# Kernel tuning notes

Measured on AMD Instinct MI355X. Metric: run time of the kernel, lower is better.

Reference implementation:

```python
import jax, jax.numpy as jnp
import numpy as np

N = 500000
D = 128
S = 4096


def setup_inputs() -> dict:
    key = jax.random.key(0)
    ks = jax.random.split(key, 8)
    x = jax.random.normal(ks[0], (N, D), dtype=jnp.float32)
    subnet_id = jax.random.randint(ks[1], (N,), 0, S, dtype=jnp.int32)
    # MLP params (Linear(D,D) x2), LayerNorm params
    lim = 1.0 / np.sqrt(D)
    W1 = jax.random.uniform(ks[2], (D, D), minval=-lim, maxval=lim, dtype=jnp.float32)
    b1 = jax.random.uniform(ks[3], (D,), minval=-lim, maxval=lim, dtype=jnp.float32)
    W2 = jax.random.uniform(ks[4], (D, D), minval=-lim, maxval=lim, dtype=jnp.float32)
    b2 = jax.random.uniform(ks[5], (D,), minval=-lim, maxval=lim, dtype=jnp.float32)
    gamma = jnp.ones((D,), dtype=jnp.float32)
    beta = jnp.zeros((D,), dtype=jnp.float32)
    return {"x": x, "subnet_id": subnet_id, "num_subnets": S,
            "W1": W1, "b1": b1, "W2": W2, "b2": b2, "gamma": gamma, "beta": beta}


def reference(x, subnet_id, num_subnets, W1, b1, W2, b2, gamma, beta):
    # scatter-mean over subnets: [S, D]
    seg_sum = jax.ops.segment_sum(x, subnet_id, num_segments=num_subnets)
    cnt = jax.ops.segment_sum(jnp.ones((x.shape[0],), x.dtype), subnet_id,
                              num_segments=num_subnets)
    mean = seg_sum / jnp.maximum(cnt, 1.0)[:, None]
    # MLP (dropout is identity in eval)
    h = jax.nn.relu(mean @ W1 + b1) @ W2 + b2
    # gather back + residual
    out = x + h[subnet_id]
    # LayerNorm (eps=1e-5)
    mu = jnp.mean(out, axis=-1, keepdims=True)
    var = jnp.var(out, axis=-1, keepdims=True)
    return (out - mu) * jax.lax.rsqrt(var + 1e-5) * gamma + beta
```

## Files before the change

kernel.cpp:

```cpp
#include <hip/hip_runtime.h>
#include <hip/hip_bf16.h>

#define DD  128
#define SS  4096
#define CAP 256

typedef float f32x4 __attribute__((ext_vector_type(4)));

static __device__ __forceinline__ void nt_store4(float* p, const float4 v) {
    f32x4 t; t[0] = v.x; t[1] = v.y; t[2] = v.z; t[3] = v.w;
    __builtin_nontemporal_store(t, (f32x4*)p);
}

__global__ void scatter_kernel(const int* __restrict__ sid,
                               int* __restrict__ fill,
                               int* __restrict__ idx, int n) {
    const int i4 = blockIdx.x * blockDim.x + threadIdx.x;
    const int n4 = n >> 2;
    if (i4 < n4) {
        int4 v = reinterpret_cast<const int4*>(sid)[i4];
        const int base = i4 * 4;
        int p;
        p = atomicAdd(&fill[v.x], 1); if (p < CAP) idx[v.x * CAP + p] = base;
        p = atomicAdd(&fill[v.y], 1); if (p < CAP) idx[v.y * CAP + p] = base + 1;
        p = atomicAdd(&fill[v.z], 1); if (p < CAP) idx[v.z * CAP + p] = base + 2;
        p = atomicAdd(&fill[v.w], 1); if (p < CAP) idx[v.w * CAP + p] = base + 3;
    }
    const int tail0 = n4 * 4;
    const int ti = tail0 + i4;
    if (ti < n && i4 < (n - tail0)) {
        int id = sid[ti];
        int p = atomicAdd(&fill[id], 1);
        if (p < CAP) idx[id * CAP + p] = ti;
    }
}

__global__ __launch_bounds__(256) void seg_mlp_kernel(
        const float* __restrict__ x,
        const int* __restrict__ idx,
        const int* __restrict__ cnt,
        const float* __restrict__ W1,
        const float* __restrict__ b1,
        const float* __restrict__ W2,
        const float* __restrict__ b2,
        float* __restrict__ h) {
    const int s    = blockIdx.x;
    const int t    = threadIdx.x;
    const int wave = t >> 6;
    const int lane = t & 63;
    const int half = lane >> 5;
    const int sub  = lane & 31;

    __shared__ int    lidx[CAP];
    __shared__ float4 part4[8][32];
    __shared__ float  m[DD];
    __shared__ float  tmp[2][DD];

    const int c  = cnt[s];
    const int cc = (c < CAP) ? c : CAP;

    if (t < cc) lidx[t] = idx[s * CAP + t];
    __syncthreads();

    const int slot = wave * 2 + half;
    const float4* x4 = reinterpret_cast<const float4*>(x);
    float4 a0 = make_float4(0.f, 0.f, 0.f, 0.f);
    float4 a1 = make_float4(0.f, 0.f, 0.f, 0.f);
    float4 a2 = make_float4(0.f, 0.f, 0.f, 0.f);
    float4 a3 = make_float4(0.f, 0.f, 0.f, 0.f);
    int j = slot;
    for (; j + 24 < cc; j += 32) {
        const int r0 = lidx[j];
        const int r1 = lidx[j + 8];
        const int r2 = lidx[j + 16];
        const int r3 = lidx[j + 24];
        float4 v0 = x4[(size_t)r0 * 32 + sub];
        float4 v1 = x4[(size_t)r1 * 32 + sub];
        float4 v2 = x4[(size_t)r2 * 32 + sub];
        float4 v3 = x4[(size_t)r3 * 32 + sub];
        a0.x += v0.x; a0.y += v0.y; a0.z += v0.z; a0.w += v0.w;
        a1.x += v1.x; a1.y += v1.y; a1.z += v1.z; a1.w += v1.w;
        a2.x += v2.x; a2.y += v2.y; a2.z += v2.z; a2.w += v2.w;
        a3.x += v3.x; a3.y += v3.y; a3.z += v3.z; a3.w += v3.w;
    }
    for (; j < cc; j += 8) {
        float4 v0 = x4[(size_t)lidx[j] * 32 + sub];
        a0.x += v0.x; a0.y += v0.y; a0.z += v0.z; a0.w += v0.w;
    }
    a0.x += a1.x + a2.x + a3.x;
    a0.y += a1.y + a2.y + a3.y;
    a0.z += a1.z + a2.z + a3.z;
    a0.w += a1.w + a2.w + a3.w;
    part4[slot][sub] = a0;
    __syncthreads();

    if (t < DD) {
        const float* pf = (const float*)part4;
        float sum = 0.f;
#pragma unroll
        for (int p = 0; p < 8; ++p) sum += pf[p * DD + t];
        m[t] = sum / fmaxf((float)c, 1.0f);
    }
    __syncthreads();

    {
        const int col = t & 127, kh = t >> 7, k0 = kh * 64;
        float a = 0.f;
        for (int k = k0; k < k0 + 64; ++k) a = fmaf(m[k], W1[k * DD + col], a);
        tmp[kh][col] = a;
    }
    __syncthreads();
    if (t < DD) m[t] = fmaxf(tmp[0][t] + tmp[1][t] + b1[t], 0.f);
    __syncthreads();

    {
        const int col = t & 127, kh = t >> 7, k0 = kh * 64;
        float a = 0.f;
        for (int k = k0; k < k0 + 64; ++k) a = fmaf(m[k], W2[k * DD + col], a);
        tmp[kh][col] = a;
    }
    __syncthreads();
    if (t < DD) h[(size_t)s * DD + t] = tmp[0][t] + tmp[1][t] + b2[t];
}

__global__ __launch_bounds__(256) void ln_kernel(
        const float* __restrict__ x,
        const int* __restrict__ sid,
        const float* __restrict__ h,
        const float* __restrict__ gamma,
        const float* __restrict__ beta,
        float* __restrict__ out,
        int n) {
    const int wave   = (blockIdx.x * blockDim.x + threadIdx.x) >> 6;
    const int lane   = threadIdx.x & 63;
    const int rrow   = lane >> 4;
    const int rsub   = lane & 15;
    const int nwaves = (gridDim.x * blockDim.x) >> 6;

    const float4* g4 = (const float4*)gamma;
    const float4* b4 = (const float4*)beta;
    const float4 ga = g4[rsub * 2],     ba = b4[rsub * 2];
    const float4 gb = g4[rsub * 2 + 1], bb = b4[rsub * 2 + 1];

    const int ngrp = n >> 2;
    for (int grp = wave; grp < ngrp; grp += nwaves) {
        const int row = grp * 4 + rrow;
        const int id  = sid[row];
        const float4* xr = (const float4*)(x + (size_t)row * DD);
        const float4* hr = (const float4*)(h + (size_t)id * DD);
        float4 o0 = xr[rsub * 2], o1 = xr[rsub * 2 + 1];
        float4 h0 = hr[rsub * 2], h1 = hr[rsub * 2 + 1];
        o0.x += h0.x; o0.y += h0.y; o0.z += h0.z; o0.w += h0.w;
        o1.x += h1.x; o1.y += h1.y; o1.z += h1.z; o1.w += h1.w;

        float sum = ((o0.x + o0.y) + (o0.z + o0.w)) +
                    ((o1.x + o1.y) + (o1.z + o1.w));
        float sq = o0.x * o0.x;
        sq = fmaf(o0.y, o0.y, sq); sq = fmaf(o0.z, o0.z, sq);
        sq = fmaf(o0.w, o0.w, sq); sq = fmaf(o1.x, o1.x, sq);
        sq = fmaf(o1.y, o1.y, sq); sq = fmaf(o1.z, o1.z, sq);
        sq = fmaf(o1.w, o1.w, sq);
#pragma unroll
        for (int off = 8; off; off >>= 1) {
            sum += __shfl_xor(sum, off);
            sq  += __shfl_xor(sq, off);
        }
        const float mu   = sum * (1.0f / DD);
        const float var  = sq * (1.0f / DD) - mu * mu;
        const float rstd = rsqrtf(var + 1e-5f);

        float4 r0, r1;
        r0.x = (o0.x - mu) * rstd * ga.x + ba.x;
        r0.y = (o0.y - mu) * rstd * ga.y + ba.y;
        r0.z = (o0.z - mu) * rstd * ga.z + ba.z;
        r0.w = (o0.w - mu) * rstd * ga.w + ba.w;
        r1.x = (o1.x - mu) * rstd * gb.x + bb.x;
        r1.y = (o1.y - mu) * rstd * gb.y + bb.y;
        r1.z = (o1.z - mu) * rstd * gb.z + bb.z;
        r1.w = (o1.w - mu) * rstd * gb.w + bb.w;
        float* orow = out + (size_t)row * DD;
        nt_store4(orow + rsub * 8,     r0);
        nt_store4(orow + rsub * 8 + 4, r1);
    }
}

extern "C" void kernel_launch(void* const* d_in, const int* in_sizes, int n_in,
                              void* d_out, int out_size, void* d_ws, size_t ws_size,
                              hipStream_t stream) {
    const float* x     = (const float*)d_in[0];
    const int*   sid   = (const int*)d_in[1];
    const float* W1    = (const float*)d_in[3];
    const float* b1    = (const float*)d_in[4];
    const float* W2    = (const float*)d_in[5];
    const float* b2    = (const float*)d_in[6];
    const float* gamma = (const float*)d_in[7];
    const float* beta  = (const float*)d_in[8];
    float*       out   = (float*)d_out;

    const int n = in_sizes[1];

    float* h    = (float*)d_ws;
    int*   fill = (int*)(h + (size_t)SS * DD);
    int*   idx  = fill + SS;

    hipMemsetAsync(fill, 0, SS * sizeof(int), stream);

    const int n4blocks = ((n >> 2) + 255) / 256 + 1;
    scatter_kernel<<<n4blocks, 256, 0, stream>>>(sid, fill, idx, n);
    seg_mlp_kernel<<<SS, 256, 0, stream>>>(x, idx, fill, W1, b1, W2, b2, h);
    ln_kernel<<<2048, 256, 0, stream>>>(x, sid, h, gamma, beta, out, n);
}
```

Before: 207.0 us.

## Split segment mean from MLP and batch eight subnets per MLP block

The fused per-subnet kernel, which read all of W1 and W2 for every one of the 4096 subnets, becomes two kernels. One computes segment means into workspace. A separate MLP kernel handles 8 subnets per block, so each weight load is reused across 8 rows held in registers. This cuts weight traffic and lets the mean kernel finish without MLP work. The cost is an extra launch and a mean round-trip through global memory, and the MLP grid has only 512 blocks of 128 threads.

```diff
diff --git a/kernel.cpp b/kernel.cpp
--- a/kernel.cpp
+++ b/kernel.cpp
@@ -35,15 +35,11 @@
     }
 }
 
-__global__ __launch_bounds__(256) void seg_mlp_kernel(
+__global__ __launch_bounds__(256) void seg_mean_kernel(
         const float* __restrict__ x,
         const int* __restrict__ idx,
         const int* __restrict__ cnt,
-        const float* __restrict__ W1,
-        const float* __restrict__ b1,
-        const float* __restrict__ W2,
-        const float* __restrict__ b2,
-        float* __restrict__ h) {
+        float* __restrict__ mean) {
     const int s    = blockIdx.x;
     const int t    = threadIdx.x;
     const int wave = t >> 6;
@@ -53,8 +49,6 @@
 
     __shared__ int    lidx[CAP];
     __shared__ float4 part4[8][32];
-    __shared__ float  m[DD];
-    __shared__ float  tmp[2][DD];
 
     const int c  = cnt[s];
     const int cc = (c < CAP) ? c : CAP;
@@ -99,28 +93,50 @@
         float sum = 0.f;
 #pragma unroll
         for (int p = 0; p < 8; ++p) sum += pf[p * DD + t];
-        m[t] = sum / fmaxf((float)c, 1.0f);
-    }
-    __syncthreads();
-
-    {
-        const int col = t & 127, kh = t >> 7, k0 = kh * 64;
-        float a = 0.f;
-        for (int k = k0; k < k0 + 64; ++k) a = fmaf(m[k], W1[k * DD + col], a);
-        tmp[kh][col] = a;
-    }
-    __syncthreads();
-    if (t < DD) m[t] = fmaxf(tmp[0][t] + tmp[1][t] + b1[t], 0.f);
-    __syncthreads();
-
-    {
-        const int col = t & 127, kh = t >> 7, k0 = kh * 64;
-        float a = 0.f;
-        for (int k = k0; k < k0 + 64; ++k) a = fmaf(m[k], W2[k * DD + col], a);
-        tmp[kh][col] = a;
-    }
-    __syncthreads();
-    if (t < DD) h[(size_t)s * DD + t] = tmp[0][t] + tmp[1][t] + b2[t];
+        mean[(size_t)s * DD + t] = sum / fmaxf((float)c, 1.0f);
+    }
+}
+
+__global__ __launch_bounds__(128) void mlp_kernel(
+        const float* __restrict__ mean,
+        const float* __restrict__ W1,
+        const float* __restrict__ b1,
+        const float* __restrict__ W2,
+        const float* __restrict__ b2,
+        float* __restrict__ h) {
+    __shared__ float m[8][DD];
+    const int t  = threadIdx.x;
+    const int s0 = blockIdx.x * 8;
+
+#pragma unroll
+    for (int r = 0; r < 8; ++r)
+        m[r][t] = mean[(size_t)(s0 + r) * DD + t];
+    __syncthreads();
+
+    float acc[8];
+    const float bv = b1[t];
+#pragma unroll
+    for (int r = 0; r < 8; ++r) acc[r] = bv;
+    for (int k = 0; k < DD; ++k) {
+        const float w = W1[k * DD + t];
+#pragma unroll
+        for (int r = 0; r < 8; ++r) acc[r] = fmaf(m[r][k], w, acc[r]);
+    }
+    __syncthreads();
+#pragma unroll
+    for (int r = 0; r < 8; ++r) m[r][t] = fmaxf(acc[r], 0.0f);
+    __syncthreads();
+
+    const float b2v = b2[t];
+#pragma unroll
+    for (int r = 0; r < 8; ++r) acc[r] = b2v;
+    for (int k = 0; k < DD; ++k) {
+        const float w = W2[k * DD + t];
+#pragma unroll
+        for (int r = 0; r < 8; ++r) acc[r] = fmaf(m[r][k], w, acc[r]);
+    }
+#pragma unroll
+    for (int r = 0; r < 8; ++r) h[(size_t)(s0 + r) * DD + t] = acc[r];
 }
 
 __global__ __launch_bounds__(256) void ln_kernel(
@@ -200,13 +216,15 @@
     const int n = in_sizes[1];
 
     float* h    = (float*)d_ws;
-    int*   fill = (int*)(h + (size_t)SS * DD);
+    float* mean = h + (size_t)SS * DD;
+    int*   fill = (int*)(mean + (size_t)SS * DD);
     int*   idx  = fill + SS;
 
     hipMemsetAsync(fill, 0, SS * sizeof(int), stream);
 
     const int n4blocks = ((n >> 2) + 255) / 256 + 1;
     scatter_kernel<<<n4blocks, 256, 0, stream>>>(sid, fill, idx, n);
-    seg_mlp_kernel<<<SS, 256, 0, stream>>>(x, idx, fill, W1, b1, W2, b2, h);
+    seg_mean_kernel<<<SS, 256, 0, stream>>>(x, idx, fill, mean);
+    mlp_kernel<<<SS / 8, DD, 0, stream>>>(mean, W1, b1, W2, b2, h);
     ln_kernel<<<2048, 256, 0, stream>>>(x, sid, h, gamma, beta, out, n);
 }
```

Result: slower. 214.6 us (+3.7%).

## Fuse scatter, segment-mean, MLP and LayerNorm into one cooperative kernel

Applied to the files above, without the earlier changes.

Replaces the memset plus three kernel launches with a single cooperative kernel of 512 blocks that uses grid-wide syncs between the phases: zeroing counts, scattering indices, segment sums, the MLP and the LayerNorm. The MLP phase now processes 4 segment rows per thread, so each W1/W2 element loaded is reused across rows. This removes launch gaps and per-kernel tail effects. In exchange it adds four grid barriers, cuts parallelism in the segment-sum phase (8 segments per block, run in sequence), adds a workspace round trip for the means, and keeps a fallback path if the cooperative launch fails.

```diff
diff --git a/kernel.cpp b/kernel.cpp
--- a/kernel.cpp
+++ b/kernel.cpp
@@ -1,15 +1,221 @@
 #include <hip/hip_runtime.h>
 #include <hip/hip_bf16.h>
-
-#define DD  128
-#define SS  4096
-#define CAP 256
+#include <hip/hip_cooperative_groups.h>
+
+namespace cg = cooperative_groups;
+
+#define DD   128
+#define SS   4096
+#define CAP  256
+#define NBLK 512
+#define NTHR 256
 
 typedef float f32x4 __attribute__((ext_vector_type(4)));
 
 static __device__ __forceinline__ void nt_store4(float* p, const float4 v) {
     f32x4 t; t[0] = v.x; t[1] = v.y; t[2] = v.z; t[3] = v.w;
     __builtin_nontemporal_store(t, (f32x4*)p);
+}
+
+__global__ __launch_bounds__(NTHR, 4) void fused_kernel(
+        const float* __restrict__ x,
+        const int*   __restrict__ sid,
+        const float* __restrict__ W1,
+        const float* __restrict__ b1,
+        const float* __restrict__ W2,
+        const float* __restrict__ b2,
+        const float* __restrict__ gamma,
+        const float* __restrict__ beta,
+        float*       __restrict__ out,
+        float*       __restrict__ h,
+        float*       __restrict__ mean,
+        int*         __restrict__ fill,
+        int*         __restrict__ idx,
+        int n) {
+    cg::grid_group grid = cg::this_grid();
+    const int t        = threadIdx.x;
+    const int gtid     = blockIdx.x * NTHR + t;
+    const int nthreads = NBLK * NTHR;
+
+    __shared__ int    lidx[CAP];
+    __shared__ float4 part4[8][32];
+    __shared__ float  mbuf[8][DD];
+
+    for (int i = gtid; i < SS; i += nthreads) fill[i] = 0;
+    grid.sync();
+
+    {
+        const int n4 = n >> 2;
+        for (int i4 = gtid; i4 < n4; i4 += nthreads) {
+            int4 v = reinterpret_cast<const int4*>(sid)[i4];
+            const int base = i4 * 4;
+            int p;
+            p = atomicAdd(&fill[v.x], 1); if (p < CAP) idx[v.x * CAP + p] = base;
+            p = atomicAdd(&fill[v.y], 1); if (p < CAP) idx[v.y * CAP + p] = base + 1;
+            p = atomicAdd(&fill[v.z], 1); if (p < CAP) idx[v.z * CAP + p] = base + 2;
+            p = atomicAdd(&fill[v.w], 1); if (p < CAP) idx[v.w * CAP + p] = base + 3;
+        }
+        const int tail0 = n4 * 4;
+        const int rem   = n - tail0;
+        if (gtid < rem) {
+            int ti = tail0 + gtid;
+            int id = sid[ti];
+            int p  = atomicAdd(&fill[id], 1);
+            if (p < CAP) idx[id * CAP + p] = ti;
+        }
+    }
+    grid.sync();
+
+    {
+        const int wave = t >> 6;
+        const int lane = t & 63;
+        const int half = lane >> 5;
+        const int sub  = lane & 31;
+        const int slot = wave * 2 + half;
+        const float4* x4 = reinterpret_cast<const float4*>(x);
+
+        for (int q = 0; q < 8; ++q) {
+            const int s  = blockIdx.x * 8 + q;
+            const int c  = fill[s];
+            const int cc = (c < CAP) ? c : CAP;
+
+            __syncthreads();
+            if (t < cc) lidx[t] = idx[s * CAP + t];
+            __syncthreads();
+
+            float4 a0 = make_float4(0.f, 0.f, 0.f, 0.f);
+            float4 a1 = make_float4(0.f, 0.f, 0.f, 0.f);
+            float4 a2 = make_float4(0.f, 0.f, 0.f, 0.f);
+            float4 a3 = make_float4(0.f, 0.f, 0.f, 0.f);
+            int j = slot;
+            for (; j + 24 < cc; j += 32) {
+                const int r0 = lidx[j];
+                const int r1 = lidx[j + 8];
+                const int r2 = lidx[j + 16];
+                const int r3 = lidx[j + 24];
+                float4 v0 = x4[(size_t)r0 * 32 + sub];
+                float4 v1 = x4[(size_t)r1 * 32 + sub];
+                float4 v2 = x4[(size_t)r2 * 32 + sub];
+                float4 v3 = x4[(size_t)r3 * 32 + sub];
+                a0.x += v0.x; a0.y += v0.y; a0.z += v0.z; a0.w += v0.w;
+                a1.x += v1.x; a1.y += v1.y; a1.z += v1.z; a1.w += v1.w;
+                a2.x += v2.x; a2.y += v2.y; a2.z += v2.z; a2.w += v2.w;
+                a3.x += v3.x; a3.y += v3.y; a3.z += v3.z; a3.w += v3.w;
+            }
+            for (; j < cc; j += 8) {
+                float4 v0 = x4[(size_t)lidx[j] * 32 + sub];
+                a0.x += v0.x; a0.y += v0.y; a0.z += v0.z; a0.w += v0.w;
+            }
+            a0.x += a1.x + a2.x + a3.x;
+            a0.y += a1.y + a2.y + a3.y;
+            a0.z += a1.z + a2.z + a3.z;
+            a0.w += a1.w + a2.w + a3.w;
+            part4[slot][sub] = a0;
+            __syncthreads();
+
+            if (t < DD) {
+                const float* pf = (const float*)part4;
+                float sum = 0.f;
+#pragma unroll
+                for (int p = 0; p < 8; ++p) sum += pf[p * DD + t];
+                mean[(size_t)s * DD + t] = sum / fmaxf((float)c, 1.0f);
+            }
+        }
+    }
+    grid.sync();
+
+    {
+        const int col = t & 127;
+        const int rb  = (t >> 7) * 4;
+        const int s0  = blockIdx.x * 8;
+
+        __syncthreads();
+#pragma unroll
+        for (int r = 0; r < 4; ++r)
+            mbuf[rb + r][col] = mean[(size_t)(s0 + rb + r) * DD + col];
+        __syncthreads();
+
+        float acc[4];
+        const float bv = b1[col];
+#pragma unroll
+        for (int r = 0; r < 4; ++r) acc[r] = bv;
+        for (int k = 0; k < DD; ++k) {
+            const float w = W1[k * DD + col];
+#pragma unroll
+            for (int r = 0; r < 4; ++r) acc[r] = fmaf(mbuf[rb + r][k], w, acc[r]);
+        }
+        __syncthreads();
+#pragma unroll
+        for (int r = 0; r < 4; ++r) mbuf[rb + r][col] = fmaxf(acc[r], 0.0f);
+        __syncthreads();
+
+        const float b2v = b2[col];
+#pragma unroll
+        for (int r = 0; r < 4; ++r) acc[r] = b2v;
+        for (int k = 0; k < DD; ++k) {
+            const float w = W2[k * DD + col];
+#pragma unroll
+            for (int r = 0; r < 4; ++r) acc[r] = fmaf(mbuf[rb + r][k], w, acc[r]);
+        }
+#pragma unroll
+        for (int r = 0; r < 4; ++r)
+            h[(size_t)(s0 + rb + r) * DD + col] = acc[r];
+    }
+    grid.sync();
+
+    {
+        const int wave   = gtid >> 6;
+        const int lane   = t & 63;
+        const int rrow   = lane >> 4;
+        const int rsub   = lane & 15;
+        const int nwaves = nthreads >> 6;
+
+        const float4* g4 = (const float4*)gamma;
+        const float4* b4 = (const float4*)beta;
+        const float4 ga = g4[rsub * 2],     ba = b4[rsub * 2];
+        const float4 gb = g4[rsub * 2 + 1], bb = b4[rsub * 2 + 1];
+
+        const int ngrp = n >> 2;
+        for (int grp = wave; grp < ngrp; grp += nwaves) {
+            const int row = grp * 4 + rrow;
+            const int id  = sid[row];
+            const float4* xr = (const float4*)(x + (size_t)row * DD);
+            const float4* hr = (const float4*)(h + (size_t)id * DD);
+            float4 o0 = xr[rsub * 2], o1 = xr[rsub * 2 + 1];
+            float4 h0 = hr[rsub * 2], h1 = hr[rsub * 2 + 1];
+            o0.x += h0.x; o0.y += h0.y; o0.z += h0.z; o0.w += h0.w;
+            o1.x += h1.x; o1.y += h1.y; o1.z += h1.z; o1.w += h1.w;
+
+            float sum = ((o0.x + o0.y) + (o0.z + o0.w)) +
+                        ((o1.x + o1.y) + (o1.z + o1.w));
+            float sq = o0.x * o0.x;
+            sq = fmaf(o0.y, o0.y, sq); sq = fmaf(o0.z, o0.z, sq);
+            sq = fmaf(o0.w, o0.w, sq); sq = fmaf(o1.x, o1.x, sq);
+            sq = fmaf(o1.y, o1.y, sq); sq = fmaf(o1.z, o1.z, sq);
+            sq = fmaf(o1.w, o1.w, sq);
+#pragma unroll
+            for (int off = 8; off; off >>= 1) {
+                sum += __shfl_xor(sum, off);
+                sq  += __shfl_xor(sq, off);
+            }
+            const float mu   = sum * (1.0f / DD);
+            const float var  = sq * (1.0f / DD) - mu * mu;
+            const float rstd = rsqrtf(var + 1e-5f);
+
+            float4 r0, r1;
+            r0.x = (o0.x - mu) * rstd * ga.x + ba.x;
+            r0.y = (o0.y - mu) * rstd * ga.y + ba.y;
+            r0.z = (o0.z - mu) * rstd * ga.z + ba.z;
+            r0.w = (o0.w - mu) * rstd * ga.w + ba.w;
+            r1.x = (o1.x - mu) * rstd * gb.x + bb.x;
+            r1.y = (o1.y - mu) * rstd * gb.y + bb.y;
+            r1.z = (o1.z - mu) * rstd * gb.z + bb.z;
+            r1.w = (o1.w - mu) * rstd * gb.w + bb.w;
+            float* orow = out + (size_t)row * DD;
+            nt_store4(orow + rsub * 8,     r0);
+            nt_store4(orow + rsub * 8 + 4, r1);
+        }
+    }
 }
 
 __global__ void scatter_kernel(const int* __restrict__ sid,
@@ -112,7 +318,6 @@
     __syncthreads();
     if (t < DD) m[t] = fmaxf(tmp[0][t] + tmp[1][t] + b1[t], 0.f);
     __syncthreads();
-
     {
         const int col = t & 127, kh = t >> 7, k0 = kh * 64;
         float a = 0.f;
@@ -197,16 +402,25 @@
     const float* beta  = (const float*)d_in[8];
     float*       out   = (float*)d_out;
 
-    const int n = in_sizes[1];
+    int n = in_sizes[1];
 
     float* h    = (float*)d_ws;
-    int*   fill = (int*)(h + (size_t)SS * DD);
+    float* mean = h + (size_t)SS * DD;
+    int*   fill = (int*)(mean + (size_t)SS * DD);
     int*   idx  = fill + SS;
 
-    hipMemsetAsync(fill, 0, SS * sizeof(int), stream);
-
-    const int n4blocks = ((n >> 2) + 255) / 256 + 1;
-    scatter_kernel<<<n4blocks, 256, 0, stream>>>(sid, fill, idx, n);
-    seg_mlp_kernel<<<SS, 256, 0, stream>>>(x, idx, fill, W1, b1, W2, b2, h);
-    ln_kernel<<<2048, 256, 0, stream>>>(x, sid, h, gamma, beta, out, n);
-}
+    void* args[] = { (void*)&x, (void*)&sid, (void*)&W1, (void*)&b1,
+                     (void*)&W2, (void*)&b2, (void*)&gamma, (void*)&beta,
+                     (void*)&out, (void*)&h, (void*)&mean, (void*)&fill,
+                     (void*)&idx, (void*)&n };
+    hipError_t err = hipLaunchCooperativeKernel((const void*)fused_kernel,
+                                                dim3(NBLK), dim3(NTHR), args,
+                                                0, stream);
+    if (err != hipSuccess) {
+        hipMemsetAsync(fill, 0, SS * sizeof(int), stream);
+        const int n4blocks = ((n >> 2) + 255) / 256 + 1;
+        scatter_kernel<<<n4blocks, 256, 0, stream>>>(sid, fill, idx, n);
+        seg_mlp_kernel<<<SS, 256, 0, stream>>>(x, idx, fill, W1, b1, W2, b2, h);
+        ln_kernel<<<2048, 256, 0, stream>>>(x, sid, h, gamma, beta, out, n);
+    }
+}
```

New measurement: 414.2 us. 100% more time.
